# Performance work log

Measured on AMD Instinct MI355X. Metric: run time of the kernel, lower is better.

Reference implementation:

```python
import jax, jax.numpy as jnp
import numpy as np

ATT = 16          # attention_size -> window = 2*ATT+1 = 33
HID = 512         # middle hidden size


def setup_inputs() -> dict:
    key = jax.random.key(0)
    ks = jax.random.split(key, 7)
    B, S, D_IN = 4, 2048, 256
    def xav(k, shape):
        fan_in, fan_out = shape[0], shape[1]
        std = np.sqrt(2.0 / (fan_in + fan_out))
        return jax.random.normal(k, shape, dtype=jnp.float32) * std
    return {
        "x": jax.random.normal(ks[0], (B, S, D_IN), dtype=jnp.float32),
        "Wq": xav(ks[1], (HID, HID)),
        "Wk": xav(ks[2], (HID, HID)),
        "Wv": xav(ks[3], (HID, HID)),
        "W0": xav(ks[4], (D_IN, HID)),
        "b0": jnp.zeros((1, 1, HID), dtype=jnp.float32),
        "W1": xav(ks[5], (HID, HID)),
        "b1": jnp.zeros((1, 1, HID), dtype=jnp.float32),
        "Wout": xav(ks[6], (HID, 2)),
        "bout": jnp.zeros((1, 1, 2), dtype=jnp.float32),
    }


def _local_windows(h, A):
    # h: [B, S, H] -> nei: [B, S, 2A+1, H], nei[b,t,j] = h[b, t+A-j] (zero padded)
    S = h.shape[1]
    padded = jnp.pad(h, ((0, 0), (A, A), (0, 0)))
    t = jnp.arange(S)[:, None]
    j = jnp.arange(2 * A + 1)[None, :]
    idx = t + 2 * A - j  # padded index of h[t + A - j]
    return padded[:, idx, :]


def reference(x, Wq, Wk, Wv, W0, b0, W1, b1, Wout, bout):
    scale = jnp.float32(np.sqrt(float(HID)))
    # pre-attention MLP layer(s)
    h = jax.nn.relu(x @ W0 + b0)                       # [B,S,H]
    nei = _local_windows(h, ATT)                       # [B,S,W,H]
    q = h @ Wq                                         # [B,S,H]
    k = nei @ Wk                                       # [B,S,W,H]
    v = nei @ Wv                                       # [B,S,W,H]
    dist = jnp.einsum('bsd,bswd->bsw', q, k) / scale   # [B,S,W]
    attn = jax.nn.softmax(dist, axis=-1)               # [B,S,W]
    ctx = jnp.einsum('bsw,bswd->bsd', attn, v)         # [B,S,H]
    # post-attention MLP layers
    h2 = jax.nn.relu(ctx @ W1 + b1)
    out = h2 @ Wout + bout                             # [B,S,2]
    return out, attn[:, :, None, :]  # attn shape [B,S,1,W] as in torch
```

## Files before the change

### kernel.cpp

```cpp
#include <hip/hip_runtime.h>

#define S_LEN 2048
#define HID 512
#define DIN 256
#define WIN 33
#define MROWS 8192
#define VTB 2080
#define VTROW 8320
#define SCALE_INV 0.04419417382415922f

typedef __attribute__((ext_vector_type(8))) short short8;
typedef __attribute__((ext_vector_type(4))) float f32x4;

__device__ __forceinline__ unsigned short f2bf(float f) {
    unsigned u = __builtin_bit_cast(unsigned, f);
    u += 0x7fffu + ((u >> 16) & 1u);
    return (unsigned short)(u >> 16);
}
__device__ __forceinline__ float bf2f(unsigned short h) {
    unsigned u = ((unsigned)h) << 16;
    return __builtin_bit_cast(float, u);
}
__device__ __forceinline__ void gl_lds16(const unsigned short* g, unsigned short* l) {
    __builtin_amdgcn_global_load_lds(
        (__attribute__((address_space(1))) unsigned int*)(g),
        (__attribute__((address_space(3))) unsigned int*)(l),
        16, 0, 0);
}

__global__ __launch_bounds__(256) void convert_bf16_kernel(
    const float* __restrict__ in, unsigned short* __restrict__ out, int n)
{
    int i = (blockIdx.x * 256 + threadIdx.x) * 4;
    if (i >= n) return;
    float4 v = *(const float4*)(in + i);
    unsigned lo = (unsigned)f2bf(v.x) | ((unsigned)f2bf(v.y) << 16);
    unsigned hi = (unsigned)f2bf(v.z) | ((unsigned)f2bf(v.w) << 16);
    uint2 p; p.x = lo; p.y = hi;
    *(uint2*)(out + i) = p;
}

__global__ void transpose_bf16_kernel(
    const float* __restrict__ in, unsigned short* __restrict__ out, int K, int N)
{
    __shared__ float tile[32][33];
    int k0 = blockIdx.x * 32, n0 = blockIdx.y * 32;
    int tx = threadIdx.x, ty = threadIdx.y;
    for (int j = 0; j < 32; j += 8)
        tile[ty + j][tx] = in[(k0 + ty + j) * N + n0 + tx];
    __syncthreads();
    for (int j = 0; j < 32; j += 8)
        out[(n0 + ty + j) * K + k0 + tx] = f2bf(tile[tx][ty + j]);
}

__global__ void transpose4_kernel(
    const float* __restrict__ wq, const float* __restrict__ wk,
    const float* __restrict__ wv, const float* __restrict__ w1,
    unsigned short* __restrict__ oq, unsigned short* __restrict__ ok,
    unsigned short* __restrict__ ov, unsigned short* __restrict__ o1)
{
    __shared__ float tile[32][33];
    const float* in; unsigned short* out;
    int z = blockIdx.z;
    if (z == 0) { in = wq; out = oq; }
    else if (z == 1) { in = wk; out = ok; }
    else if (z == 2) { in = wv; out = ov; }
    else { in = w1; out = o1; }
    int k0 = blockIdx.x * 32, n0 = blockIdx.y * 32;
    int tx = threadIdx.x, ty = threadIdx.y;
    for (int j = 0; j < 32; j += 8)
        tile[ty + j][tx] = in[(k0 + ty + j) * HID + n0 + tx];
    __syncthreads();
    for (int j = 0; j < 32; j += 8)
        out[(n0 + ty + j) * HID + k0 + tx] = f2bf(tile[tx][ty + j]);
}

__global__ void vt_pad_kernel(unsigned short* __restrict__ Vt)
{
    int v = blockIdx.x;
    int tid = threadIdx.x;
    int b = tid >> 5, p = tid & 31;
    int off = (p < 16) ? p : (2048 + p);
    Vt[(size_t)v * VTROW + b * VTB + off] = 0;
}

template<int K, int MODE>
__global__ __launch_bounds__(256) void gemm128_kernel(
    const unsigned short* __restrict__ A,
    const unsigned short* __restrict__ Bt,
    const float* __restrict__ bias,
    unsigned short* __restrict__ C0,
    unsigned short* __restrict__ C1,
    unsigned short* __restrict__ C2)
{
    __shared__ __align__(16) unsigned short Al[4][128][8];
    __shared__ __align__(16) unsigned short Bl[4][128][8];
    const int tid = threadIdx.x;
    const int lane = tid & 63, wid = tid >> 6;
    const int bm = blockIdx.x, bn = blockIdx.y;
    const int wr = wid >> 1, wc = wid & 1;
    const int r16 = lane & 15, kq = lane >> 4;

    f32x4 acc[4][4] = {};

    const int c0 = tid, c1 = tid + 256;
    const unsigned short* aS0 = A + (size_t)(bm * 128 + (c0 & 127)) * K + (c0 >> 7) * 8;
    const unsigned short* aS1 = A + (size_t)(bm * 128 + (c1 & 127)) * K + (c1 >> 7) * 8;
    const unsigned short* bS0 = Bt + (size_t)(bn * 128 + (c0 & 127)) * K + (c0 >> 7) * 8;
    const unsigned short* bS1 = Bt + (size_t)(bn * 128 + (c1 & 127)) * K + (c1 >> 7) * 8;
    unsigned short* aD0 = &Al[0][0][0] + c0 * 8;
    unsigned short* aD1 = &Al[0][0][0] + c1 * 8;
    unsigned short* bD0 = &Bl[0][0][0] + c0 * 8;
    unsigned short* bD1 = &Bl[0][0][0] + c1 * 8;

    for (int kt = 0; kt < K / 32; ++kt) {
        gl_lds16(aS0 + kt * 32, aD0);
        gl_lds16(aS1 + kt * 32, aD1);
        gl_lds16(bS0 + kt * 32, bD0);
        gl_lds16(bS1 + kt * 32, bD1);
        __syncthreads();
        short8 af[4], bfr[4];
        #pragma unroll
        for (int mi = 0; mi < 4; ++mi) af[mi] = *(const short8*)&Al[kq][wr * 64 + mi * 16 + r16][0];
        #pragma unroll
        for (int ni = 0; ni < 4; ++ni) bfr[ni] = *(const short8*)&Bl[kq][wc * 64 + ni * 16 + r16][0];
        #pragma unroll
        for (int mi = 0; mi < 4; ++mi)
            #pragma unroll
            for (int ni = 0; ni < 4; ++ni)
                acc[mi][ni] = __builtin_amdgcn_mfma_f32_16x16x32_bf16(af[mi], bfr[ni], acc[mi][ni], 0, 0, 0);
        __syncthreads();
    }

    if constexpr (MODE == 0) {
        #pragma unroll
        for (int mi = 0; mi < 4; ++mi) {
            int row0 = bm * 128 + wr * 64 + mi * 16 + kq * 4;
            #pragma unroll
            for (int ni = 0; ni < 4; ++ni) {
                int col = bn * 128 + wc * 64 + ni * 16 + r16;
                float bv = bias[col];
                #pragma unroll
                for (int r = 0; r < 4; ++r) {
                    float v = fmaxf(acc[mi][ni][r] + bv, 0.0f);
                    C0[(size_t)(row0 + r) * HID + col] = f2bf(v);
                }
            }
        }
    } else {
        if (bn < 8) {
            unsigned short* dst = (bn < 4) ? C0 : C1;
            int cb = (bn & 3) * 128 + wc * 64;
            #pragma unroll
            for (int mi = 0; mi < 4; ++mi) {
                int row0 = bm * 128 + wr * 64 + mi * 16 + kq * 4;
                #pragma unroll
                for (int ni = 0; ni < 4; ++ni) {
                    int col = cb + ni * 16 + r16;
                    #pragma unroll
                    for (int r = 0; r < 4; ++r)
                        dst[(size_t)(row0 + r) * HID + col] = f2bf(acc[mi][ni][r]);
                }
            }
        } else {
            #pragma unroll
            for (int mi = 0; mi < 4; ++mi) {
                int t = bm * 128 + wr * 64 + mi * 16 + kq * 4;
                int bb = t >> 11, tl = t & 2047;
                #pragma unroll
                for (int ni = 0; ni < 4; ++ni) {
                    int v = (bn - 8) * 128 + wc * 64 + ni * 16 + r16;
                    unsigned lo = (unsigned)f2bf(acc[mi][ni][0]) | ((unsigned)f2bf(acc[mi][ni][1]) << 16);
                    unsigned hi = (unsigned)f2bf(acc[mi][ni][2]) | ((unsigned)f2bf(acc[mi][ni][3]) << 16);
                    uint2 pk; pk.x = lo; pk.y = hi;
                    *(uint2*)(C2 + (size_t)v * VTROW + bb * VTB + 16 + tl) = pk;
                }
            }
        }
    }
}

__global__ __launch_bounds__(256) void attn_kernel(
    const unsigned short* __restrict__ Qb,
    const unsigned short* __restrict__ Kb,
    const unsigned short* __restrict__ Vt,
    float* __restrict__ attn_out,
    unsigned short* __restrict__ ctx)
{
    __shared__ __align__(16) float Sl[4][32][68];
    __shared__ __align__(16) unsigned short Pl[32 * 64];
    const int tid = threadIdx.x;
    const int lane = tid & 63;
    const int w = tid >> 6;
    const int t0g = blockIdx.x * 32;
    const int b = t0g >> 11;
    const int t0 = t0g & 2047;
    const int r16 = lane & 15, kq = lane >> 4;

    f32x4 s[2][4] = {};
    const unsigned short* qbase = Qb + (size_t)t0g * HID + w * 128 + kq * 8;
    const unsigned short* kbase = Kb + (long)(t0g - 16) * HID + w * 128 + kq * 8;
    #pragma unroll
    for (int ks = 0; ks < 4; ++ks) {
        short8 a0 = *(const short8*)(qbase + (size_t)r16 * HID + ks * 32);
        short8 a1 = *(const short8*)(qbase + (size_t)(16 + r16) * HID + ks * 32);
        #pragma unroll
        for (int ni = 0; ni < 4; ++ni) {
            short8 bf = *(const short8*)(kbase + (size_t)(ni * 16 + r16) * HID + ks * 32);
            s[0][ni] = __builtin_amdgcn_mfma_f32_16x16x32_bf16(a0, bf, s[0][ni], 0, 0, 0);
            s[1][ni] = __builtin_amdgcn_mfma_f32_16x16x32_bf16(a1, bf, s[1][ni], 0, 0, 0);
        }
    }
    #pragma unroll
    for (int mi = 0; mi < 2; ++mi)
        #pragma unroll
        for (int ni = 0; ni < 4; ++ni)
            #pragma unroll
            for (int r = 0; r < 4; ++r)
                Sl[w][mi * 16 + kq * 4 + r][ni * 16 + r16] = s[mi][ni][r];
    __syncthreads();

    {
        const int i = tid >> 3;
        const int c8 = (tid & 7) * 8;
        float sv[8];
        #pragma unroll
        for (int cc = 0; cc < 8; ++cc) {
            float a = Sl[0][i][c8 + cc] + Sl[1][i][c8 + cc]
                    + Sl[2][i][c8 + cc] + Sl[3][i][c8 + cc];
            int m = c8 + cc;
            bool inb = (m >= i) && (m <= i + 32);
            int krow = t0 + m - 16;
            bool inseq = (krow >= 0) && (krow < S_LEN);
            sv[cc] = inb ? (inseq ? a * SCALE_INV : 0.0f) : -INFINITY;
        }
        float mx = sv[0];
        #pragma unroll
        for (int cc = 1; cc < 8; ++cc) mx = fmaxf(mx, sv[cc]);
        mx = fmaxf(mx, __shfl_xor(mx, 1));
        mx = fmaxf(mx, __shfl_xor(mx, 2));
        mx = fmaxf(mx, __shfl_xor(mx, 4));
        float es = 0.0f;
        #pragma unroll
        for (int cc = 0; cc < 8; ++cc) { sv[cc] = __expf(sv[cc] - mx); es += sv[cc]; }
        es += __shfl_xor(es, 1);
        es += __shfl_xor(es, 2);
        es += __shfl_xor(es, 4);
        float inv = 1.0f / es;
        unsigned short pb[8];
        #pragma unroll
        for (int cc = 0; cc < 8; ++cc) {
            float p = sv[cc] * inv;
            pb[cc] = f2bf(p);
            int m = c8 + cc;
            if (m >= i && m <= i + 32)
                attn_out[(size_t)(t0g + i) * WIN + (i + 32 - m)] = p;
        }
        uint4 pk;
        pk.x = (unsigned)pb[0] | ((unsigned)pb[1] << 16);
        pk.y = (unsigned)pb[2] | ((unsigned)pb[3] << 16);
        pk.z = (unsigned)pb[4] | ((unsigned)pb[5] << 16);
        pk.w = (unsigned)pb[6] | ((unsigned)pb[7] << 16);
        *(uint4*)((char*)Pl + i * 128 + ((c8 * 2) ^ ((i & 7) << 4))) = pk;
    }
    __syncthreads();

    f32x4 c[2][8] = {};
    const char* plb = (const char*)Pl;
    const unsigned short* vtb = Vt + (size_t)b * VTB + t0;
    #pragma unroll
    for (int ks = 0; ks < 2; ++ks) {
        int cb = ks * 64 + kq * 16;
        short8 a0 = *(const short8*)(plb + r16 * 128 + (cb ^ ((r16 & 7) << 4)));
        short8 a1 = *(const short8*)(plb + (16 + r16) * 128 + (cb ^ ((r16 & 7) << 4)));
        #pragma unroll
        for (int nd = 0; nd < 8; ++nd) {
            const unsigned short* vp = vtb + (size_t)(w * 128 + nd * 16 + r16) * VTROW + ks * 32 + kq * 8;
            short8 bf = *(const short8*)vp;
            c[0][nd] = __builtin_amdgcn_mfma_f32_16x16x32_bf16(a0, bf, c[0][nd], 0, 0, 0);
            c[1][nd] = __builtin_amdgcn_mfma_f32_16x16x32_bf16(a1, bf, c[1][nd], 0, 0, 0);
        }
    }
    #pragma unroll
    for (int mi = 0; mi < 2; ++mi) {
        int row0 = t0g + mi * 16 + kq * 4;
        #pragma unroll
        for (int nd = 0; nd < 8; ++nd) {
            int col = w * 128 + nd * 16 + r16;
            #pragma unroll
            for (int r = 0; r < 4; ++r)
                ctx[(size_t)(row0 + r) * HID + col] = f2bf(c[mi][nd][r]);
        }
    }
}

__global__ __launch_bounds__(256) void final_kernel(
    const unsigned short* __restrict__ h2,
    const float* __restrict__ Wout,
    const float* __restrict__ bout,
    float* __restrict__ out)
{
    int wid = blockIdx.x * 4 + (threadIdx.x >> 6);
    int lane = threadIdx.x & 63;
    const unsigned short* hr = h2 + (size_t)wid * HID;
    float a0 = 0.0f, a1 = 0.0f;
    for (int i = 0; i < 4; ++i) {
        int d0 = i * 128 + 2 * lane;
        unsigned u = *(const unsigned*)(hr + d0);
        float hx = bf2f((unsigned short)u), hy = bf2f((unsigned short)(u >> 16));
        float2 w0 = *(const float2*)(Wout + d0 * 2);
        float2 w1 = *(const float2*)(Wout + d0 * 2 + 2);
        a0 += hx * w0.x + hy * w1.x;
        a1 += hx * w0.y + hy * w1.y;
    }
    for (int off = 32; off > 0; off >>= 1) {
        a0 += __shfl_xor(a0, off);
        a1 += __shfl_xor(a1, off);
    }
    if (lane == 0) {
        out[(size_t)wid * 2]     = a0 + bout[0];
        out[(size_t)wid * 2 + 1] = a1 + bout[1];
    }
}

extern "C" void kernel_launch(void* const* d_in, const int* in_sizes, int n_in,
                              void* d_out, int out_size, void* d_ws, size_t ws_size,
                              hipStream_t stream)
{
    const float* x    = (const float*)d_in[0];
    const float* Wq   = (const float*)d_in[1];
    const float* Wk   = (const float*)d_in[2];
    const float* Wv   = (const float*)d_in[3];
    const float* W0   = (const float*)d_in[4];
    const float* b0   = (const float*)d_in[5];
    const float* W1   = (const float*)d_in[6];
    const float* b1   = (const float*)d_in[7];
    const float* Wout = (const float*)d_in[8];
    const float* bout = (const float*)d_in[9];

    char* ws = (char*)d_ws;
    unsigned short* xb    = (unsigned short*)(ws + 0);
    unsigned short* Wt0   = (unsigned short*)(ws + (4u  << 20));
    unsigned short* Wtqkv = (unsigned short*)(ws + 4456448u);
    unsigned short* Wt1   = (unsigned short*)(ws + 6029312u);
    unsigned short* hB    = (unsigned short*)(ws + (8u  << 20));
    unsigned short* Qb    = (unsigned short*)(ws + (16u << 20));
    unsigned short* Kb    = (unsigned short*)(ws + (24u << 20));
    unsigned short* Vt    = (unsigned short*)(ws + (32u << 20));
    unsigned short* ctxB  = (unsigned short*)(ws + (41u << 20));
    unsigned short* h2B   = (unsigned short*)(ws + (50u << 20));

    float* outp  = (float*)d_out;
    float* attnp = (float*)d_out + MROWS * 2;

    convert_bf16_kernel<<<2048, 256, 0, stream>>>(x, xb, MROWS * DIN);

    dim3 tb(32, 8);
    transpose_bf16_kernel<<<dim3(DIN / 32, HID / 32), tb, 0, stream>>>(W0, Wt0, DIN, HID);
    transpose4_kernel<<<dim3(16, 16, 4), tb, 0, stream>>>(
        Wq, Wk, Wv, W1,
        Wtqkv, Wtqkv + 512 * 512, Wtqkv + 2 * 512 * 512, Wt1);

    vt_pad_kernel<<<512, 128, 0, stream>>>(Vt);

    gemm128_kernel<DIN, 0><<<dim3(64, 4), 256, 0, stream>>>(xb, Wt0, b0, hB, nullptr, nullptr);

    gemm128_kernel<HID, 1><<<dim3(64, 12), 256, 0, stream>>>(hB, Wtqkv, nullptr, Qb, Kb, Vt);

    attn_kernel<<<256, 256, 0, stream>>>(Qb, Kb, Vt, attnp, ctxB);

    gemm128_kernel<HID, 0><<<dim3(64, 4), 256, 0, stream>>>(ctxB, Wt1, b1, h2B, nullptr, nullptr);

    final_kernel<<<2048, 256, 0, stream>>>(h2B, Wout, bout, outp);
}
```

Before: 156.5 us.

## Merge prep kernels, fuse output projection into last GEMM, stage V transpose via LDS

Folds the x conversion, weight transposes, Vt padding and output-bias initialisation into one prep kernel, cutting four launches to one. The final Wout projection moves into the epilogue of the W1 GEMM: each block reduces its column slice with shuffles and atomically adds into the bias-initialised output, so h2 is never written and final_kernel goes away. The V-transpose epilogue now stages tiles in swizzled LDS so it can issue 16-byte coalesced stores instead of scattered 8-byte ones. The attention score padding also shrinks from 68 to 66 columns. Atomics make the output sum order nondeterministic and add contention across the four column blocks.

```diff
diff --git a/kernel.cpp b/kernel.cpp
--- a/kernel.cpp
+++ b/kernel.cpp
@@ -28,60 +28,54 @@
         16, 0, 0);
 }
 
-__global__ __launch_bounds__(256) void convert_bf16_kernel(
-    const float* __restrict__ in, unsigned short* __restrict__ out, int n)
-{
-    int i = (blockIdx.x * 256 + threadIdx.x) * 4;
-    if (i >= n) return;
-    float4 v = *(const float4*)(in + i);
-    unsigned lo = (unsigned)f2bf(v.x) | ((unsigned)f2bf(v.y) << 16);
-    unsigned hi = (unsigned)f2bf(v.z) | ((unsigned)f2bf(v.w) << 16);
-    uint2 p; p.x = lo; p.y = hi;
-    *(uint2*)(out + i) = p;
-}
-
-__global__ void transpose_bf16_kernel(
-    const float* __restrict__ in, unsigned short* __restrict__ out, int K, int N)
+__global__ __launch_bounds__(256) void prep_kernel(
+    const float* __restrict__ x,
+    const float* __restrict__ Wq, const float* __restrict__ Wk,
+    const float* __restrict__ Wv, const float* __restrict__ W0,
+    const float* __restrict__ W1, const float* __restrict__ bout,
+    unsigned short* __restrict__ xb, unsigned short* __restrict__ Wt0,
+    unsigned short* __restrict__ Wtqkv, unsigned short* __restrict__ Wt1,
+    unsigned short* __restrict__ Vt, float* __restrict__ outp)
 {
     __shared__ float tile[32][33];
-    int k0 = blockIdx.x * 32, n0 = blockIdx.y * 32;
-    int tx = threadIdx.x, ty = threadIdx.y;
-    for (int j = 0; j < 32; j += 8)
-        tile[ty + j][tx] = in[(k0 + ty + j) * N + n0 + tx];
-    __syncthreads();
-    for (int j = 0; j < 32; j += 8)
-        out[(n0 + ty + j) * K + k0 + tx] = f2bf(tile[tx][ty + j]);
-}
-
-__global__ void transpose4_kernel(
-    const float* __restrict__ wq, const float* __restrict__ wk,
-    const float* __restrict__ wv, const float* __restrict__ w1,
-    unsigned short* __restrict__ oq, unsigned short* __restrict__ ok,
-    unsigned short* __restrict__ ov, unsigned short* __restrict__ o1)
-{
-    __shared__ float tile[32][33];
-    const float* in; unsigned short* out;
-    int z = blockIdx.z;
-    if (z == 0) { in = wq; out = oq; }
-    else if (z == 1) { in = wk; out = ok; }
-    else if (z == 2) { in = wv; out = ov; }
-    else { in = w1; out = o1; }
-    int k0 = blockIdx.x * 32, n0 = blockIdx.y * 32;
-    int tx = threadIdx.x, ty = threadIdx.y;
-    for (int j = 0; j < 32; j += 8)
-        tile[ty + j][tx] = in[(k0 + ty + j) * HID + n0 + tx];
-    __syncthreads();
-    for (int j = 0; j < 32; j += 8)
-        out[(n0 + ty + j) * HID + k0 + tx] = f2bf(tile[tx][ty + j]);
-}
-
-__global__ void vt_pad_kernel(unsigned short* __restrict__ Vt)
-{
-    int v = blockIdx.x;
-    int tid = threadIdx.x;
-    int b = tid >> 5, p = tid & 31;
-    int off = (p < 16) ? p : (2048 + p);
-    Vt[(size_t)v * VTROW + b * VTB + off] = 0;
+    const int blk = blockIdx.x, tid = threadIdx.x;
+    if (blk < 2048) {
+        int i = (blk * 256 + tid) * 4;
+        float4 v = *(const float4*)(x + i);
+        unsigned lo = (unsigned)f2bf(v.x) | ((unsigned)f2bf(v.y) << 16);
+        unsigned hi = (unsigned)f2bf(v.z) | ((unsigned)f2bf(v.w) << 16);
+        uint2 p; p.x = lo; p.y = hi;
+        *(uint2*)(xb + i) = p;
+    } else if (blk < 2064) {
+        int i = ((blk - 2048) * 256 + tid) * 4;
+        float4 o; o.x = bout[0]; o.y = bout[1]; o.z = bout[0]; o.w = bout[1];
+        *(float4*)(outp + i) = o;
+    } else if (blk < 2320) {
+        int t = (blk - 2064) * 256 + tid;
+        int v = t >> 7, s = t & 127;
+        int b = s >> 5, p = s & 31;
+        int off = (p < 16) ? p : (2048 + p);
+        Vt[(size_t)v * VTROW + b * VTB + off] = 0;
+    } else {
+        int tt = blk - 2320;
+        const float* in; unsigned short* out; int K, kt, nt;
+        if (tt < 128) { in = W0; out = Wt0; K = DIN; kt = tt & 7; nt = tt >> 3; }
+        else {
+            int z = (tt - 128) >> 8, r = (tt - 128) & 255;
+            kt = r & 15; nt = r >> 4; K = HID;
+            if (z == 0)      { in = Wq; out = Wtqkv; }
+            else if (z == 1) { in = Wk; out = Wtqkv + 512 * 512; }
+            else if (z == 2) { in = Wv; out = Wtqkv + 2 * 512 * 512; }
+            else             { in = W1; out = Wt1; }
+        }
+        int k0 = kt * 32, n0 = nt * 32;
+        int tx = tid & 31, ty = tid >> 5;
+        for (int j = 0; j < 32; j += 8)
+            tile[ty + j][tx] = in[(size_t)(k0 + ty + j) * HID + n0 + tx];
+        __syncthreads();
+        for (int j = 0; j < 32; j += 8)
+            out[(size_t)(n0 + ty + j) * K + k0 + tx] = f2bf(tile[tx][ty + j]);
+    }
 }
 
 template<int K, int MODE>
@@ -91,10 +85,11 @@
     const float* __restrict__ bias,
     unsigned short* __restrict__ C0,
     unsigned short* __restrict__ C1,
-    unsigned short* __restrict__ C2)
+    unsigned short* __restrict__ C2,
+    const float* __restrict__ Wout,
+    float* __restrict__ outp)
 {
-    __shared__ __align__(16) unsigned short Al[4][128][8];
-    __shared__ __align__(16) unsigned short Bl[4][128][8];
+    __shared__ __align__(16) unsigned short SMEM[8192];
     const int tid = threadIdx.x;
     const int lane = tid & 63, wid = tid >> 6;
     const int bm = blockIdx.x, bn = blockIdx.y;
@@ -108,10 +103,10 @@
     const unsigned short* aS1 = A + (size_t)(bm * 128 + (c1 & 127)) * K + (c1 >> 7) * 8;
     const unsigned short* bS0 = Bt + (size_t)(bn * 128 + (c0 & 127)) * K + (c0 >> 7) * 8;
     const unsigned short* bS1 = Bt + (size_t)(bn * 128 + (c1 & 127)) * K + (c1 >> 7) * 8;
-    unsigned short* aD0 = &Al[0][0][0] + c0 * 8;
-    unsigned short* aD1 = &Al[0][0][0] + c1 * 8;
-    unsigned short* bD0 = &Bl[0][0][0] + c0 * 8;
-    unsigned short* bD1 = &Bl[0][0][0] + c1 * 8;
+    unsigned short* aD0 = SMEM + c0 * 8;
+    unsigned short* aD1 = SMEM + c1 * 8;
+    unsigned short* bD0 = SMEM + 4096 + c0 * 8;
+    unsigned short* bD1 = SMEM + 4096 + c1 * 8;
 
     for (int kt = 0; kt < K / 32; ++kt) {
         gl_lds16(aS0 + kt * 32, aD0);
@@ -121,9 +116,11 @@
         __syncthreads();
         short8 af[4], bfr[4];
         #pragma unroll
-        for (int mi = 0; mi < 4; ++mi) af[mi] = *(const short8*)&Al[kq][wr * 64 + mi * 16 + r16][0];
-        #pragma unroll
-        for (int ni = 0; ni < 4; ++ni) bfr[ni] = *(const short8*)&Bl[kq][wc * 64 + ni * 16 + r16][0];
+        for (int mi = 0; mi < 4; ++mi)
+            af[mi] = *(const short8*)(SMEM + kq * 1024 + (wr * 64 + mi * 16 + r16) * 8);
+        #pragma unroll
+        for (int ni = 0; ni < 4; ++ni)
+            bfr[ni] = *(const short8*)(SMEM + 4096 + kq * 1024 + (wc * 64 + ni * 16 + r16) * 8);
         #pragma unroll
         for (int mi = 0; mi < 4; ++mi)
             #pragma unroll
@@ -147,7 +144,7 @@
                 }
             }
         }
-    } else {
+    } else if constexpr (MODE == 1) {
         if (bn < 8) {
             unsigned short* dst = (bn < 4) ? C0 : C1;
             int cb = (bn & 3) * 128 + wc * 64;
@@ -163,19 +160,70 @@
                 }
             }
         } else {
-            #pragma unroll
-            for (int mi = 0; mi < 4; ++mi) {
-                int t = bm * 128 + wr * 64 + mi * 16 + kq * 4;
-                int bb = t >> 11, tl = t & 2047;
-                #pragma unroll
-                for (int ni = 0; ni < 4; ++ni) {
-                    int v = (bn - 8) * 128 + wc * 64 + ni * 16 + r16;
-                    unsigned lo = (unsigned)f2bf(acc[mi][ni][0]) | ((unsigned)f2bf(acc[mi][ni][1]) << 16);
-                    unsigned hi = (unsigned)f2bf(acc[mi][ni][2]) | ((unsigned)f2bf(acc[mi][ni][3]) << 16);
-                    uint2 pk; pk.x = lo; pk.y = hi;
-                    *(uint2*)(C2 + (size_t)v * VTROW + bb * VTB + 16 + tl) = pk;
-                }
+            const int bb  = (bm * 128) >> 11;
+            const int tl0 = (bm * 128) & 2047;
+            #pragma unroll
+            for (int p = 0; p < 2; ++p) {
+                if (wc == p) {
+                    #pragma unroll
+                    for (int mi = 0; mi < 4; ++mi) {
+                        int ttw = wr * 64 + mi * 16 + kq * 4;
+                        #pragma unroll
+                        for (int ni = 0; ni < 4; ++ni) {
+                            int vv = ni * 16 + r16;
+                            unsigned lo = (unsigned)f2bf(acc[mi][ni][0]) | ((unsigned)f2bf(acc[mi][ni][1]) << 16);
+                            unsigned hi = (unsigned)f2bf(acc[mi][ni][2]) | ((unsigned)f2bf(acc[mi][ni][3]) << 16);
+                            uint2 pk; pk.x = lo; pk.y = hi;
+                            *(uint2*)&SMEM[vv * 128 + (ttw ^ ((vv & 7) << 3))] = pk;
+                        }
+                    }
+                }
+                __syncthreads();
+                #pragma unroll
+                for (int it = 0; it < 4; ++it) {
+                    int vv  = (tid >> 4) + it * 16;
+                    int tt8 = (tid & 15) * 8;
+                    uint4 q = *(const uint4*)&SMEM[vv * 128 + (tt8 ^ ((vv & 7) << 3))];
+                    int vg = (bn - 8) * 128 + p * 64 + vv;
+                    *(uint4*)(C2 + (size_t)vg * VTROW + bb * VTB + 16 + tl0 + tt8) = q;
+                }
+                __syncthreads();
             }
+        }
+    } else {
+        float o0[16], o1[16];
+        #pragma unroll
+        for (int t2 = 0; t2 < 16; ++t2) { o0[t2] = 0.0f; o1[t2] = 0.0f; }
+        #pragma unroll
+        for (int ni = 0; ni < 4; ++ni) {
+            int col = bn * 128 + wc * 64 + ni * 16 + r16;
+            float bv = bias[col];
+            float2 wv = *(const float2*)(Wout + col * 2);
+            #pragma unroll
+            for (int mi = 0; mi < 4; ++mi)
+                #pragma unroll
+                for (int r = 0; r < 4; ++r) {
+                    float v = fmaxf(acc[mi][ni][r] + bv, 0.0f);
+                    o0[mi * 4 + r] += v * wv.x;
+                    o1[mi * 4 + r] += v * wv.y;
+                }
+        }
+        #pragma unroll
+        for (int s = 1; s < 16; s <<= 1)
+            #pragma unroll
+            for (int t2 = 0; t2 < 16; ++t2) {
+                o0[t2] += __shfl_xor(o0[t2], s);
+                o1[t2] += __shfl_xor(o1[t2], s);
+            }
+        if (r16 == 0) {
+            #pragma unroll
+            for (int mi = 0; mi < 4; ++mi)
+                #pragma unroll
+                for (int r = 0; r < 4; ++r) {
+                    int row = bm * 128 + wr * 64 + mi * 16 + kq * 4 + r;
+                    atomicAdd(&outp[(size_t)row * 2],     o0[mi * 4 + r]);
+                    atomicAdd(&outp[(size_t)row * 2 + 1], o1[mi * 4 + r]);
+                }
         }
     }
 }
@@ -187,7 +235,7 @@
     float* __restrict__ attn_out,
     unsigned short* __restrict__ ctx)
 {
-    __shared__ __align__(16) float Sl[4][32][68];
+    __shared__ __align__(16) float Sl[4][32][66];
     __shared__ __align__(16) unsigned short Pl[32 * 64];
     const int tid = threadIdx.x;
     const int lane = tid & 63;
@@ -291,35 +339,6 @@
             for (int r = 0; r < 4; ++r)
                 ctx[(size_t)(row0 + r) * HID + col] = f2bf(c[mi][nd][r]);
         }
-    }
-}
-
-__global__ __launch_bounds__(256) void final_kernel(
-    const unsigned short* __restrict__ h2,
-    const float* __restrict__ Wout,
-    const float* __restrict__ bout,
-    float* __restrict__ out)
-{
-    int wid = blockIdx.x * 4 + (threadIdx.x >> 6);
-    int lane = threadIdx.x & 63;
-    const unsigned short* hr = h2 + (size_t)wid * HID;
-    float a0 = 0.0f, a1 = 0.0f;
-    for (int i = 0; i < 4; ++i) {
-        int d0 = i * 128 + 2 * lane;
-        unsigned u = *(const unsigned*)(hr + d0);
-        float hx = bf2f((unsigned short)u), hy = bf2f((unsigned short)(u >> 16));
-        float2 w0 = *(const float2*)(Wout + d0 * 2);
-        float2 w1 = *(const float2*)(Wout + d0 * 2 + 2);
-        a0 += hx * w0.x + hy * w1.x;
-        a1 += hx * w0.y + hy * w1.y;
-    }
-    for (int off = 32; off > 0; off >>= 1) {
-        a0 += __shfl_xor(a0, off);
-        a1 += __shfl_xor(a1, off);
-    }
-    if (lane == 0) {
-        out[(size_t)wid * 2]     = a0 + bout[0];
-        out[(size_t)wid * 2 + 1] = a1 + bout[1];
     }
 }
 
@@ -348,28 +367,21 @@
     unsigned short* Kb    = (unsigned short*)(ws + (24u << 20));
     unsigned short* Vt    = (unsigned short*)(ws + (32u << 20));
     unsigned short* ctxB  = (unsigned short*)(ws + (41u << 20));
-    unsigned short* h2B   = (unsigned short*)(ws + (50u << 20));
 
     float* outp  = (float*)d_out;
     float* attnp = (float*)d_out + MROWS * 2;
 
-    convert_bf16_kernel<<<2048, 256, 0, stream>>>(x, xb, MROWS * DIN);
-
-    dim3 tb(32, 8);
-    transpose_bf16_kernel<<<dim3(DIN / 32, HID / 32), tb, 0, stream>>>(W0, Wt0, DIN, HID);
-    transpose4_kernel<<<dim3(16, 16, 4), tb, 0, stream>>>(
-        Wq, Wk, Wv, W1,
-        Wtqkv, Wtqkv + 512 * 512, Wtqkv + 2 * 512 * 512, Wt1);
-
-    vt_pad_kernel<<<512, 128, 0, stream>>>(Vt);
-
-    gemm128_kernel<DIN, 0><<<dim3(64, 4), 256, 0, stream>>>(xb, Wt0, b0, hB, nullptr, nullptr);
-
-    gemm128_kernel<HID, 1><<<dim3(64, 12), 256, 0, stream>>>(hB, Wtqkv, nullptr, Qb, Kb, Vt);
+    prep_kernel<<<3472, 256, 0, stream>>>(x, Wq, Wk, Wv, W0, W1, bout,
+                                          xb, Wt0, Wtqkv, Wt1, Vt, outp);
+
+    gemm128_kernel<DIN, 0><<<dim3(64, 4), 256, 0, stream>>>(
+        xb, Wt0, b0, hB, nullptr, nullptr, nullptr, nullptr);
+
+    gemm128_kernel<HID, 1><<<dim3(64, 12), 256, 0, stream>>>(
+        hB, Wtqkv, nullptr, Qb, Kb, Vt, nullptr, nullptr);
 
     attn_kernel<<<256, 256, 0, stream>>>(Qb, Kb, Vt, attnp, ctxB);
 
-    gemm128_kernel<HID, 0><<<dim3(64, 4), 256, 0, stream>>>(ctxB, Wt1, b1, h2B, nullptr, nullptr);
-
-    final_kernel<<<2048, 256, 0, stream>>>(h2B, Wout, bout, outp);
-}
+    gemm128_kernel<HID, 2><<<dim3(64, 4), 256, 0, stream>>>(
+        ctxB, Wt1, b1, nullptr, nullptr, nullptr, Wout, outp);
+}
```

Result: no change. 155.1 us (-0.9%).
